# Optimization experiments

Hardware: AMD Instinct MI355X
Metric: run time of the kernel (lower is better)

Reference implementation:

```python
import jax, jax.numpy as jnp
import numpy as np

HID = 64      # HIDDEN_DIM
VOCAB = 64    # VOCAB_SIZE
INNER = 24    # INNER_DIM
SEQ = 32      # SEQ_LEN
CAP = 8       # CAPACITY_LIMIT (deque maxlen)
LR = 0.05     # INFERENCE_LR
B1, B2, EPS = 0.9, 0.999, 1e-8   # torch Adam defaults
LN_EPS = 1e-5                    # torch LayerNorm default
BATCH = 8192


def setup_inputs() -> dict:
    key = jax.random.key(0)
    ks = jax.random.split(key, 8)
    def w(k, shape, s=0.02):
        return jax.random.normal(k, shape, jnp.float32) * s
    return {
        "seqs": jax.random.randint(ks[0], (BATCH, SEQ), 0, VOCAB, dtype=jnp.int32),
        "embed": w(ks[1], (VOCAB, HID), 1.0),
        "ff_w1": w(ks[2], (HID, 2 * HID)), "ff_b1": jnp.zeros((2 * HID,), jnp.float32),
        "ff_w2": w(ks[3], (2 * HID, HID)), "ff_b2": jnp.zeros((HID,), jnp.float32),
        "ln_g": jnp.ones((HID,), jnp.float32), "ln_b": jnp.zeros((HID,), jnp.float32),
        "mlp_w1": w(ks[4], (HID, INNER), 0.1), "mlp_b1": jnp.zeros((INNER,), jnp.float32),
        "mlp_w2": w(ks[5], (INNER, HID), 0.1), "mlp_b2": jnp.zeros((HID,), jnp.float32),
        "out_w": w(ks[6], (HID, VOCAB)), "out_b": jnp.zeros((VOCAB,), jnp.float32),
    }


def _mlp(p, x):
    w1, b1, w2, b2 = p
    return jnp.maximum(x @ w1 + b1, 0.0) @ w2 + b2


def reference(seqs, embed, ff_w1, ff_b1, ff_w2, ff_b2, ln_g, ln_b,
              mlp_w1, mlp_b1, mlp_w2, mlp_b2, out_w, out_b):
    # Encoder over all tokens used (t = 0..SEQ-2), batched: [B, 31, HID]
    h = embed[seqs[:, : SEQ - 1]]
    f = jnp.maximum(h @ ff_w1 + ff_b1, 0.0) @ ff_w2 + ff_b2
    x = h + f
    mu = x.mean(-1, keepdims=True)
    var = ((x - mu) ** 2).mean(-1, keepdims=True)
    enc = ln_g * (x - mu) * jax.lax.rsqrt(var + LN_EPS) + ln_b

    # deque(maxlen=8) over pairs (t even -> key, t odd -> val) keeps last 8 pairs:
    # keys at t = 14,16,...,28 ; vals at t = 15,17,...,29. Entries are detached.
    keys = jax.lax.stop_gradient(enc[:, 14:29:2])  # [B, 8, HID]
    vals = jax.lax.stop_gradient(enc[:, 15:30:2])  # [B, 8, HID]
    q = enc[:, SEQ - 2]                            # [B, HID]

    # load_state_dict copy breaks the graph -> base MLP params are constants here
    p0 = tuple(jax.lax.stop_gradient(p) for p in (mlp_w1, mlp_b1, mlp_w2, mlp_b2))
    steps = jnp.arange(1, CAP + 1, dtype=jnp.float32)

    def per_sample(k_i, v_i, q_i):
        def adam_step(carry, kv):
            p, m, v = carry
            kh, vh, t = kv
            g = jax.grad(lambda pp: jnp.mean((_mlp(pp, kh) - vh) ** 2))(p)
            m = jax.tree_util.tree_map(lambda a, b: B1 * a + (1.0 - B1) * b, m, g)
            v = jax.tree_util.tree_map(lambda a, b: B2 * a + (1.0 - B2) * b * b, v, g)
            bc1 = 1.0 - B1 ** t
            bc2 = 1.0 - B2 ** t
            p = jax.tree_util.tree_map(
                lambda pp, mm, vv: pp - LR * (mm / bc1) / (jnp.sqrt(vv / bc2) + EPS),
                p, m, v)
            return (p, m, v), None
        zeros = jax.tree_util.tree_map(jnp.zeros_like, p0)
        (pT, _, _), _ = jax.lax.scan(adam_step, (p0, zeros, zeros), (k_i, v_i, steps))
        return _mlp(pT, q_i)

    hq = jax.vmap(per_sample)(keys, vals, q)   # [B, HID]
    return hq @ out_w + out_b                  # [B, VOCAB]
```

## Files before the change

### kernel.cpp

```cpp
#include <hip/hip_runtime.h>
#include <hip/hip_bf16.h>
#include <math.h>

#define HID   64
#define VOCABN 64
#define INNER 24
#define SEQN  32
#define CAPN  8
#define NPOS  17
#define BATCHN 8192

typedef float f32x4 __attribute__((ext_vector_type(4)));
typedef float f32x2 __attribute__((ext_vector_type(2)));

static __device__ __forceinline__ f32x2 pk_fma2(f32x2 a, f32x2 b, f32x2 c) {
  f32x2 r; r.x = fmaf(a.x, b.x, c.x); r.y = fmaf(a.y, b.y, c.y); return r;
}
static __device__ __forceinline__ f32x2 pk_max2(f32x2 a, f32x2 b) {
  f32x2 r; r.x = fmaxf(a.x, b.x); r.y = fmaxf(a.y, b.y); return r;
}
static __device__ __forceinline__ f32x2 sp2(float x) { return (f32x2){x, x}; }

static __device__ const float CMSBR[8] = {
  0.01581139f, 0.01176584f, 0.01010053f, 0.00918844f,
  0.00862495f, 0.00825540f, 0.00800653f, 0.00783856f
};

__device__ __forceinline__ float allred32(float x) {
  int y;
  y = __builtin_amdgcn_update_dpp(__float_as_int(x), __float_as_int(x),
                                  0xB1, 0xF, 0xF, false);
  x += __int_as_float(y);
  y = __builtin_amdgcn_update_dpp(__float_as_int(x), __float_as_int(x),
                                  0x4E, 0xF, 0xF, false);
  x += __int_as_float(y);
  x += __int_as_float(__builtin_amdgcn_ds_swizzle(__float_as_int(x), 0x101F));
  x += __int_as_float(__builtin_amdgcn_ds_swizzle(__float_as_int(x), 0x201F));
  x += __int_as_float(__builtin_amdgcn_ds_swizzle(__float_as_int(x), 0x401F));
  return x;
}

__global__ __launch_bounds__(128) void build_table(
    const float* __restrict__ embed,
    const float* __restrict__ ff_w1,
    const float* __restrict__ ff_b1,
    const float* __restrict__ ff_w2,
    const float* __restrict__ ff_b2,
    const float* __restrict__ ln_g,
    const float* __restrict__ ln_b,
    float* __restrict__ etab)
{
  __shared__ float h[64];
  __shared__ float A1[128];
  __shared__ float xs[64];
  const int r = blockIdx.x;
  const int t = threadIdx.x;

  if (t < 64) h[t] = embed[r * 64 + t];
  __syncthreads();

  {
    float acc = ff_b1[t];
    #pragma unroll 8
    for (int k = 0; k < 64; ++k)
      acc = fmaf(h[k], ff_w1[k * 128 + t], acc);
    A1[t] = fmaxf(acc, 0.f);
  }
  __syncthreads();

  if (t < 64) {
    float acc = ff_b2[t];
    #pragma unroll 8
    for (int k = 0; k < 128; ++k)
      acc = fmaf(A1[k], ff_w2[k * 64 + t], acc);
    xs[t] = acc + h[t];
  }
  __syncthreads();

  if (t < 64) {
    float s1 = 0.f;
    if (t < 4)
      for (int j = 0; j < 16; ++j) s1 += xs[t + 4 * j];
    s1 += __shfl_xor(s1, 1);
    s1 += __shfl_xor(s1, 2);
    s1 = __shfl(s1, 0);
    float mu = s1 * 0.015625f;

    float s2 = 0.f;
    if (t < 4)
      for (int j = 0; j < 16; ++j) {
        float d = xs[t + 4 * j] - mu;
        s2 = fmaf(d, d, s2);
      }
    s2 += __shfl_xor(s2, 1);
    s2 += __shfl_xor(s2, 2);
    s2 = __shfl(s2, 0);
    float var = s2 * 0.015625f;
    float rs  = rsqrtf(var + 1e-5f);

    etab[r * 64 + t] = fmaf((xs[t] - mu) * rs, ln_g[t], ln_b[t]);
  }
}

__device__ __forceinline__ void adam_pk(f32x2& p, f32x2& m, f32x2& v,
                                        f32x2 g1, f32x2 g2, float cmsbr) {
  m = pk_fma2(sp2(0.9f),   m, g1);
  v = pk_fma2(sp2(0.999f), v, g2);
  f32x2 vc = pk_max2(v, sp2(1e-30f));
  f32x2 r; r.x = __builtin_amdgcn_rsqf(vc.x); r.y = __builtin_amdgcn_rsqf(vc.y);
  f32x2 t = m * sp2(cmsbr);
  p = pk_fma2(-t, r, p);
}

__global__ __launch_bounds__(256, 2) void adapt_kernel(
    const int* __restrict__ seqs,
    const float* __restrict__ etab,
    const float* __restrict__ mlp_w1,
    const float* __restrict__ mlp_b1,
    const float* __restrict__ mlp_w2,
    const float* __restrict__ mlp_b2,
    const float* __restrict__ out_w,
    const float* __restrict__ out_b,
    float* __restrict__ out)
{
  __shared__ __align__(16) float hqv[4][64];
  const int t    = threadIdx.x;
  const int wv   = t >> 6;
  const int lane = t & 63;
  const int h    = lane >> 5;
  const int u    = lane & 31;
  const int s    = blockIdx.x * 4 + wv;
  const int off  = 12 * h;

  const int* __restrict__ srow = seqs + s * SEQN + 14;

  f32x2 w1[12], m1[12], v1[12], w2[12], m2[12], v2[12];
  #pragma unroll
  for (int m = 0; m < 12; ++m) {
    f32x2 a; a.x = mlp_w1[(2 * u) * INNER + off + m];
             a.y = mlp_w1[(2 * u + 1) * INNER + off + m];
    w1[m] = a;
    w2[m] = *(const f32x2*)&mlp_w2[(off + m) * HID + 2 * u];
    m1[m] = sp2(0.f); v1[m] = sp2(0.f); m2[m] = sp2(0.f); v2[m] = sp2(0.f);
  }
  const bool own1 = (u < 6);
  f32x2 b1v = own1 ? *(const f32x2*)&mlp_b1[off + 2 * u] : sp2(0.f);
  f32x2 mb1 = sp2(0.f), vb1 = sp2(0.f);
  f32x2 b2v = (h == 0) ? *(const f32x2*)&mlp_b2[2 * u] : sp2(0.f);
  f32x2 mb2 = sp2(0.f), vb2 = sp2(0.f);

  const bool ou0 = (u == 0), ou1 = (u == 1), ou2 = (u == 2);
  const bool ou3 = (u == 3), ou4 = (u == 4), ou5 = (u == 5);

  const f32x2* e2 = (const f32x2*)etab;
  f32x2 kp = e2[srow[0] * 32 + u];
  f32x2 vp = e2[srow[1] * 32 + u];

  #pragma unroll 1
  for (int st = 0; st < 8; ++st) {
    const float cmsbr = CMSBR[st];

    f32x2 pz[12];
    #pragma unroll
    for (int m = 0; m < 12; ++m) pz[m] = kp * w1[m];
    pz[0].x  += ou0 ? b1v.x : 0.f;  pz[1].y  += ou0 ? b1v.y : 0.f;
    pz[2].x  += ou1 ? b1v.x : 0.f;  pz[3].y  += ou1 ? b1v.y : 0.f;
    pz[4].x  += ou2 ? b1v.x : 0.f;  pz[5].y  += ou2 ? b1v.y : 0.f;
    pz[6].x  += ou3 ? b1v.x : 0.f;  pz[7].y  += ou3 ? b1v.y : 0.f;
    pz[8].x  += ou4 ? b1v.x : 0.f;  pz[9].y  += ou4 ? b1v.y : 0.f;
    pz[10].x += ou5 ? b1v.x : 0.f;  pz[11].y += ou5 ? b1v.y : 0.f;
    float a_[12];
    #pragma unroll
    for (int m = 0; m < 12; ++m) a_[m] = allred32(pz[m].x + pz[m].y);
    #pragma unroll
    for (int m = 0; m < 12; ++m) a_[m] = fmaxf(a_[m], 0.f);

    f32x2 qA = (h == 0) ? b2v : sp2(0.f);
    #pragma unroll
    for (int m = 0; m < 6; ++m)  qA = pk_fma2(sp2(a_[m]), w2[m], qA);
    f32x2 qB = sp2(0.f);
    #pragma unroll
    for (int m = 6; m < 12; ++m) qB = pk_fma2(sp2(a_[m]), w2[m], qB);
    f32x2 sH = qA + qB;
    f32x2 sO; sO.x = __shfl_xor(sH.x, 32); sO.y = __shfl_xor(sH.y, 32);
    f32x2 ys  = sH + sO;
    f32x2 dyv = (ys - vp) * sp2(0.03125f);

    int pp1 = 2 * st + 2; pp1 = pp1 < 16 ? pp1 : 16;
    int pp2 = 2 * st + 3; pp2 = pp2 < 16 ? pp2 : 16;
    f32x2 kn = e2[srow[pp1] * 32 + u];
    f32x2 vn = e2[srow[pp2] * 32 + u];

    float dz[12];
    #pragma unroll
    for (int m = 0; m < 12; ++m) {
      f32x2 bb = w2[m] * dyv;
      dz[m] = allred32(bb.x + bb.y);
    }
    #pragma unroll
    for (int m = 0; m < 12; ++m) dz[m] = (a_[m] > 0.f) ? dz[m] : 0.f;

    f32x2 k01  = kp * sp2(0.1f);
    f32x2 ksq  = (sp2(0.001f) * kp) * kp;
    f32x2 dy01 = dyv * sp2(0.1f);
    f32x2 dysq = (sp2(0.001f) * dyv) * dyv;
    #pragma unroll
    for (int m = 0; m < 12; ++m) {
      float dzs = dz[m] * dz[m];
      adam_pk(w1[m], m1[m], v1[m], k01 * sp2(dz[m]), ksq * sp2(dzs), cmsbr);
      float as = a_[m] * a_[m];
      adam_pk(w2[m], m2[m], v2[m], dy01 * sp2(a_[m]), dysq * sp2(as), cmsbr);
    }
    float glo = ou0 ? dz[0] : ou1 ? dz[2] : ou2 ? dz[4]
              : ou3 ? dz[6] : ou4 ? dz[8] : dz[10];
    float ghi = ou0 ? dz[1] : ou1 ? dz[3] : ou2 ? dz[5]
              : ou3 ? dz[7] : ou4 ? dz[9] : dz[11];
    f32x2 g1b; g1b.x = 0.1f * glo;           g1b.y = 0.1f * ghi;
    f32x2 g2b; g2b.x = 0.001f * (glo * glo); g2b.y = 0.001f * (ghi * ghi);
    adam_pk(b1v, mb1, vb1, g1b, g2b, cmsbr);
    adam_pk(b2v, mb2, vb2, dy01, dysq, cmsbr);

    kp = kn; vp = vn;
  }

  {
    f32x2 pz[12];
    #pragma unroll
    for (int m = 0; m < 12; ++m) pz[m] = kp * w1[m];
    pz[0].x  += ou0 ? b1v.x : 0.f;  pz[1].y  += ou0 ? b1v.y : 0.f;
    pz[2].x  += ou1 ? b1v.x : 0.f;  pz[3].y  += ou1 ? b1v.y : 0.f;
    pz[4].x  += ou2 ? b1v.x : 0.f;  pz[5].y  += ou2 ? b1v.y : 0.f;
    pz[6].x  += ou3 ? b1v.x : 0.f;  pz[7].y  += ou3 ? b1v.y : 0.f;
    pz[8].x  += ou4 ? b1v.x : 0.f;  pz[9].y  += ou4 ? b1v.y : 0.f;
    pz[10].x += ou5 ? b1v.x : 0.f;  pz[11].y += ou5 ? b1v.y : 0.f;
    float aq[12];
    #pragma unroll
    for (int m = 0; m < 12; ++m) aq[m] = fmaxf(allred32(pz[m].x + pz[m].y), 0.f);
    f32x2 qA = (h == 0) ? b2v : sp2(0.f);
    #pragma unroll
    for (int m = 0; m < 6; ++m)  qA = pk_fma2(sp2(aq[m]), w2[m], qA);
    f32x2 qB = sp2(0.f);
    #pragma unroll
    for (int m = 6; m < 12; ++m) qB = pk_fma2(sp2(aq[m]), w2[m], qB);
    f32x2 sH = qA + qB;
    f32x2 sO; sO.x = __shfl_xor(sH.x, 32); sO.y = __shfl_xor(sH.y, 32);
    f32x2 hq = sH + sO;
    if (h == 0) *(f32x2*)&hqv[wv][2 * u] = hq;
  }
  __syncthreads();

  {
    float acc = out_b[lane];
    const f32x4* hv = (const f32x4*)hqv[wv];
    #pragma unroll
    for (int j4 = 0; j4 < 16; ++j4) {
      f32x4 h4 = hv[j4];
      acc = fmaf(h4.x, out_w[(4 * j4 + 0) * 64 + lane], acc);
      acc = fmaf(h4.y, out_w[(4 * j4 + 1) * 64 + lane], acc);
      acc = fmaf(h4.z, out_w[(4 * j4 + 2) * 64 + lane], acc);
      acc = fmaf(h4.w, out_w[(4 * j4 + 3) * 64 + lane], acc);
    }
    out[(size_t)s * 64 + lane] = acc;
  }
}

extern "C" void kernel_launch(void* const* d_in, const int* in_sizes, int n_in,
                              void* d_out, int out_size, void* d_ws, size_t ws_size,
                              hipStream_t stream) {
  const int*   seqs   = (const int*)d_in[0];
  const float* embed  = (const float*)d_in[1];
  const float* ff_w1  = (const float*)d_in[2];
  const float* ff_b1  = (const float*)d_in[3];
  const float* ff_w2  = (const float*)d_in[4];
  const float* ff_b2  = (const float*)d_in[5];
  const float* ln_g   = (const float*)d_in[6];
  const float* ln_b   = (const float*)d_in[7];
  const float* mlp_w1 = (const float*)d_in[8];
  const float* mlp_b1 = (const float*)d_in[9];
  const float* mlp_w2 = (const float*)d_in[10];
  const float* mlp_b2 = (const float*)d_in[11];
  const float* out_w  = (const float*)d_in[12];
  const float* out_b  = (const float*)d_in[13];

  float* etab = (float*)d_ws;

  build_table<<<64, 128, 0, stream>>>(
      embed, ff_w1, ff_b1, ff_w2, ff_b2, ln_g, ln_b, etab);
  adapt_kernel<<<BATCHN / 4, 256, 0, stream>>>(
      seqs, etab, mlp_w1, mlp_b1, mlp_w2, mlp_b2, out_w, out_b,
      (float*)d_out);
}
```

Baseline: 179.7 us.

## Remap wave work to four 16-lane groups each owning 4 hidden elements

Changes the per-sample wave decomposition from two 32-lane halves (2 hidden elements per lane, 12 inner units each) to four 16-lane groups (4 hidden elements per lane, 6 inner units each). Each cross-lane reduction now spans 16 lanes instead of 32, dropping one swizzle step per reduction and halving the number of reductions per lane. The output recombination needs an extra swizzle plus shuffle across groups, and bias ownership logic becomes more intricate. Per-lane register state for Adam stays about the same.

```diff
diff --git a/kernel.cpp b/kernel.cpp
--- a/kernel.cpp
+++ b/kernel.cpp
@@ -13,20 +13,32 @@
 typedef float f32x4 __attribute__((ext_vector_type(4)));
 typedef float f32x2 __attribute__((ext_vector_type(2)));
 
-static __device__ __forceinline__ f32x2 pk_fma2(f32x2 a, f32x2 b, f32x2 c) {
-  f32x2 r; r.x = fmaf(a.x, b.x, c.x); r.y = fmaf(a.y, b.y, c.y); return r;
-}
-static __device__ __forceinline__ f32x2 pk_max2(f32x2 a, f32x2 b) {
-  f32x2 r; r.x = fmaxf(a.x, b.x); r.y = fmaxf(a.y, b.y); return r;
-}
-static __device__ __forceinline__ f32x2 sp2(float x) { return (f32x2){x, x}; }
+static __device__ __forceinline__ f32x4 sp4(float x) { return (f32x4){x, x, x, x}; }
+static __device__ __forceinline__ f32x4 fma4(f32x4 a, f32x4 b, f32x4 c) {
+  f32x4 r; r.x = fmaf(a.x, b.x, c.x); r.y = fmaf(a.y, b.y, c.y);
+           r.z = fmaf(a.z, b.z, c.z); r.w = fmaf(a.w, b.w, c.w); return r;
+}
+static __device__ __forceinline__ f32x4 max4(f32x4 a, float b) {
+  f32x4 r; r.x = fmaxf(a.x, b); r.y = fmaxf(a.y, b);
+           r.z = fmaxf(a.z, b); r.w = fmaxf(a.w, b); return r;
+}
+static __device__ __forceinline__ f32x4 rsq4(f32x4 a) {
+  f32x4 r; r.x = __builtin_amdgcn_rsqf(a.x); r.y = __builtin_amdgcn_rsqf(a.y);
+           r.z = __builtin_amdgcn_rsqf(a.z); r.w = __builtin_amdgcn_rsqf(a.w); return r;
+}
 
 static __device__ const float CMSBR[8] = {
   0.01581139f, 0.01176584f, 0.01010053f, 0.00918844f,
   0.00862495f, 0.00825540f, 0.00800653f, 0.00783856f
 };
 
-__device__ __forceinline__ float allred32(float x) {
+template <int PAT>
+static __device__ __forceinline__ float swz(float x) {
+  return __int_as_float(__builtin_amdgcn_ds_swizzle(__float_as_int(x), PAT));
+}
+
+__device__ __forceinline__ float allred16q(f32x4 p) {
+  float x = (p.x + p.y) + (p.z + p.w);
   int y;
   y = __builtin_amdgcn_update_dpp(__float_as_int(x), __float_as_int(x),
                                   0xB1, 0xF, 0xF, false);
@@ -34,9 +46,8 @@
   y = __builtin_amdgcn_update_dpp(__float_as_int(x), __float_as_int(x),
                                   0x4E, 0xF, 0xF, false);
   x += __int_as_float(y);
-  x += __int_as_float(__builtin_amdgcn_ds_swizzle(__float_as_int(x), 0x101F));
-  x += __int_as_float(__builtin_amdgcn_ds_swizzle(__float_as_int(x), 0x201F));
-  x += __int_as_float(__builtin_amdgcn_ds_swizzle(__float_as_int(x), 0x401F));
+  x += swz<0x101F>(x);
+  x += swz<0x201F>(x);
   return x;
 }
 
@@ -102,14 +113,13 @@
   }
 }
 
-__device__ __forceinline__ void adam_pk(f32x2& p, f32x2& m, f32x2& v,
-                                        f32x2 g1, f32x2 g2, float cmsbr) {
-  m = pk_fma2(sp2(0.9f),   m, g1);
-  v = pk_fma2(sp2(0.999f), v, g2);
-  f32x2 vc = pk_max2(v, sp2(1e-30f));
-  f32x2 r; r.x = __builtin_amdgcn_rsqf(vc.x); r.y = __builtin_amdgcn_rsqf(vc.y);
-  f32x2 t = m * sp2(cmsbr);
-  p = pk_fma2(-t, r, p);
+__device__ __forceinline__ void adam_q(f32x4& p, f32x4& m, f32x4& v,
+                                       f32x4 g1, f32x4 g2, float cmsbr) {
+  m = fma4(sp4(0.9f),   m, g1);
+  v = fma4(sp4(0.999f), v, g2);
+  f32x4 r = rsq4(max4(v, 1e-30f));
+  f32x4 t = m * sp4(cmsbr);
+  p = fma4(-t, r, p);
 }
 
 __global__ __launch_bounds__(256, 2) void adapt_kernel(
@@ -127,125 +137,142 @@
   const int t    = threadIdx.x;
   const int wv   = t >> 6;
   const int lane = t & 63;
-  const int h    = lane >> 5;
-  const int u    = lane & 31;
+  const int g    = lane >> 4;
+  const int u16  = lane & 15;
   const int s    = blockIdx.x * 4 + wv;
-  const int off  = 12 * h;
+  const int off  = 6 * g;
 
   const int* __restrict__ srow = seqs + s * SEQN + 14;
 
-  f32x2 w1[12], m1[12], v1[12], w2[12], m2[12], v2[12];
+  f32x4 w1q[6], m1q[6], v1q[6], w2q[6], m2q[6], v2q[6];
   #pragma unroll
-  for (int m = 0; m < 12; ++m) {
-    f32x2 a; a.x = mlp_w1[(2 * u) * INNER + off + m];
-             a.y = mlp_w1[(2 * u + 1) * INNER + off + m];
-    w1[m] = a;
-    w2[m] = *(const f32x2*)&mlp_w2[(off + m) * HID + 2 * u];
-    m1[m] = sp2(0.f); v1[m] = sp2(0.f); m2[m] = sp2(0.f); v2[m] = sp2(0.f);
-  }
-  const bool own1 = (u < 6);
-  f32x2 b1v = own1 ? *(const f32x2*)&mlp_b1[off + 2 * u] : sp2(0.f);
-  f32x2 mb1 = sp2(0.f), vb1 = sp2(0.f);
-  f32x2 b2v = (h == 0) ? *(const f32x2*)&mlp_b2[2 * u] : sp2(0.f);
-  f32x2 mb2 = sp2(0.f), vb2 = sp2(0.f);
-
-  const bool ou0 = (u == 0), ou1 = (u == 1), ou2 = (u == 2);
-  const bool ou3 = (u == 3), ou4 = (u == 4), ou5 = (u == 5);
-
-  const f32x2* e2 = (const f32x2*)etab;
-  f32x2 kp = e2[srow[0] * 32 + u];
-  f32x2 vp = e2[srow[1] * 32 + u];
+  for (int m = 0; m < 6; ++m) {
+    f32x4 a;
+    a.x = mlp_w1[(4 * u16 + 0) * INNER + off + m];
+    a.y = mlp_w1[(4 * u16 + 1) * INNER + off + m];
+    a.z = mlp_w1[(4 * u16 + 2) * INNER + off + m];
+    a.w = mlp_w1[(4 * u16 + 3) * INNER + off + m];
+    w1q[m] = a;
+    w2q[m] = *(const f32x4*)&mlp_w2[(off + m) * HID + 4 * u16];
+    m1q[m] = sp4(0.f); v1q[m] = sp4(0.f); m2q[m] = sp4(0.f); v2q[m] = sp4(0.f);
+  }
+  f32x4 b1q = sp4(0.f);
+  if (!(g & 1)) {
+    if (u16 == 0) { b1q.x = mlp_b1[off + 0]; b1q.y = mlp_b1[off + 1];
+                    b1q.z = mlp_b1[off + 2]; b1q.w = mlp_b1[off + 3]; }
+    else if (u16 == 1) { b1q.x = mlp_b1[off + 4]; b1q.y = mlp_b1[off + 5]; }
+  } else {
+    if (u16 == 1) { b1q.z = mlp_b1[off + 0]; b1q.w = mlp_b1[off + 1]; }
+    else if (u16 == 2) { b1q.x = mlp_b1[off + 2]; b1q.y = mlp_b1[off + 3];
+                         b1q.z = mlp_b1[off + 4]; b1q.w = mlp_b1[off + 5]; }
+  }
+  f32x4 mb1 = sp4(0.f), vb1 = sp4(0.f);
+  f32x4 b2q = *(const f32x4*)&mlp_b2[4 * u16];
+  f32x4 mb2 = sp4(0.f), vb2 = sp4(0.f);
+
+  const bool ge0 = !(g & 1) && (u16 == 0);
+  const bool ge1 = !(g & 1) && (u16 == 1);
+  const bool go1 =  (g & 1) && (u16 == 1);
+  const bool go2 =  (g & 1) && (u16 == 2);
+  const bool g0a = (g == 0);
+
+  const f32x4* e4 = (const f32x4*)etab;
+  f32x4 kp = e4[srow[0] * 16 + u16];
+  f32x4 vp = e4[srow[1] * 16 + u16];
 
   #pragma unroll 1
   for (int st = 0; st < 8; ++st) {
     const float cmsbr = CMSBR[st];
 
-    f32x2 pz[12];
-    #pragma unroll
-    for (int m = 0; m < 12; ++m) pz[m] = kp * w1[m];
-    pz[0].x  += ou0 ? b1v.x : 0.f;  pz[1].y  += ou0 ? b1v.y : 0.f;
-    pz[2].x  += ou1 ? b1v.x : 0.f;  pz[3].y  += ou1 ? b1v.y : 0.f;
-    pz[4].x  += ou2 ? b1v.x : 0.f;  pz[5].y  += ou2 ? b1v.y : 0.f;
-    pz[6].x  += ou3 ? b1v.x : 0.f;  pz[7].y  += ou3 ? b1v.y : 0.f;
-    pz[8].x  += ou4 ? b1v.x : 0.f;  pz[9].y  += ou4 ? b1v.y : 0.f;
-    pz[10].x += ou5 ? b1v.x : 0.f;  pz[11].y += ou5 ? b1v.y : 0.f;
-    float a_[12];
-    #pragma unroll
-    for (int m = 0; m < 12; ++m) a_[m] = allred32(pz[m].x + pz[m].y);
-    #pragma unroll
-    for (int m = 0; m < 12; ++m) a_[m] = fmaxf(a_[m], 0.f);
-
-    f32x2 qA = (h == 0) ? b2v : sp2(0.f);
-    #pragma unroll
-    for (int m = 0; m < 6; ++m)  qA = pk_fma2(sp2(a_[m]), w2[m], qA);
-    f32x2 qB = sp2(0.f);
-    #pragma unroll
-    for (int m = 6; m < 12; ++m) qB = pk_fma2(sp2(a_[m]), w2[m], qB);
-    f32x2 sH = qA + qB;
-    f32x2 sO; sO.x = __shfl_xor(sH.x, 32); sO.y = __shfl_xor(sH.y, 32);
-    f32x2 ys  = sH + sO;
-    f32x2 dyv = (ys - vp) * sp2(0.03125f);
+    f32x4 pz[6];
+    #pragma unroll
+    for (int m = 0; m < 6; ++m) pz[m] = kp * w1q[m];
+    pz[0].x += ge0 ? b1q.x : 0.f;  pz[0].z += go1 ? b1q.z : 0.f;
+    pz[1].y += ge0 ? b1q.y : 0.f;  pz[1].w += go1 ? b1q.w : 0.f;
+    pz[2].z += ge0 ? b1q.z : 0.f;  pz[2].x += go2 ? b1q.x : 0.f;
+    pz[3].w += ge0 ? b1q.w : 0.f;  pz[3].y += go2 ? b1q.y : 0.f;
+    pz[4].x += ge1 ? b1q.x : 0.f;  pz[4].z += go2 ? b1q.z : 0.f;
+    pz[5].y += ge1 ? b1q.y : 0.f;  pz[5].w += go2 ? b1q.w : 0.f;
+    float a_[6];
+    #pragma unroll
+    for (int m = 0; m < 6; ++m) a_[m] = allred16q(pz[m]);
+    #pragma unroll
+    for (int m = 0; m < 6; ++m) a_[m] = fmaxf(a_[m], 0.f);
+
+    f32x4 yq;
+    yq.x = g0a ? b2q.x : 0.f; yq.y = g0a ? b2q.y : 0.f;
+    yq.z = g0a ? b2q.z : 0.f; yq.w = g0a ? b2q.w : 0.f;
+    #pragma unroll
+    for (int m = 0; m < 6; ++m) yq = fma4(sp4(a_[m]), w2q[m], yq);
+    { f32x4 e; e.x = swz<0x401F>(yq.x); e.y = swz<0x401F>(yq.y);
+               e.z = swz<0x401F>(yq.z); e.w = swz<0x401F>(yq.w);
+      yq = yq + e; }
+    { f32x4 e; e.x = __shfl_xor(yq.x, 32); e.y = __shfl_xor(yq.y, 32);
+               e.z = __shfl_xor(yq.z, 32); e.w = __shfl_xor(yq.w, 32);
+      yq = yq + e; }
+    f32x4 dyq = (yq - vp) * sp4(0.03125f);
 
     int pp1 = 2 * st + 2; pp1 = pp1 < 16 ? pp1 : 16;
     int pp2 = 2 * st + 3; pp2 = pp2 < 16 ? pp2 : 16;
-    f32x2 kn = e2[srow[pp1] * 32 + u];
-    f32x2 vn = e2[srow[pp2] * 32 + u];
-
-    float dz[12];
-    #pragma unroll
-    for (int m = 0; m < 12; ++m) {
-      f32x2 bb = w2[m] * dyv;
-      dz[m] = allred32(bb.x + bb.y);
+    f32x4 kn = e4[srow[pp1] * 16 + u16];
+    f32x4 vn = e4[srow[pp2] * 16 + u16];
+
+    float dz[6];
+    #pragma unroll
+    for (int m = 0; m < 6; ++m) dz[m] = allred16q(w2q[m] * dyq);
+    #pragma unroll
+    for (int m = 0; m < 6; ++m) dz[m] = (a_[m] > 0.f) ? dz[m] : 0.f;
+
+    f32x4 k01  = kp * sp4(0.1f);
+    f32x4 ksq  = (sp4(0.001f) * kp) * kp;
+    f32x4 dy01 = dyq * sp4(0.1f);
+    f32x4 dysq = (sp4(0.001f) * dyq) * dyq;
+    #pragma unroll
+    for (int m = 0; m < 6; ++m) {
+      float dzs = dz[m] * dz[m];
+      adam_q(w1q[m], m1q[m], v1q[m], k01 * sp4(dz[m]), ksq * sp4(dzs), cmsbr);
+      float as = a_[m] * a_[m];
+      adam_q(w2q[m], m2q[m], v2q[m], dy01 * sp4(a_[m]), dysq * sp4(as), cmsbr);
     }
-    #pragma unroll
-    for (int m = 0; m < 12; ++m) dz[m] = (a_[m] > 0.f) ? dz[m] : 0.f;
-
-    f32x2 k01  = kp * sp2(0.1f);
-    f32x2 ksq  = (sp2(0.001f) * kp) * kp;
-    f32x2 dy01 = dyv * sp2(0.1f);
-    f32x2 dysq = (sp2(0.001f) * dyv) * dyv;
-    #pragma unroll
-    for (int m = 0; m < 12; ++m) {
-      float dzs = dz[m] * dz[m];
-      adam_pk(w1[m], m1[m], v1[m], k01 * sp2(dz[m]), ksq * sp2(dzs), cmsbr);
-      float as = a_[m] * a_[m];
-      adam_pk(w2[m], m2[m], v2[m], dy01 * sp2(a_[m]), dysq * sp2(as), cmsbr);
-    }
-    float glo = ou0 ? dz[0] : ou1 ? dz[2] : ou2 ? dz[4]
-              : ou3 ? dz[6] : ou4 ? dz[8] : dz[10];
-    float ghi = ou0 ? dz[1] : ou1 ? dz[3] : ou2 ? dz[5]
-              : ou3 ? dz[7] : ou4 ? dz[9] : dz[11];
-    f32x2 g1b; g1b.x = 0.1f * glo;           g1b.y = 0.1f * ghi;
-    f32x2 g2b; g2b.x = 0.001f * (glo * glo); g2b.y = 0.001f * (ghi * ghi);
-    adam_pk(b1v, mb1, vb1, g1b, g2b, cmsbr);
-    adam_pk(b2v, mb2, vb2, dy01, dysq, cmsbr);
+    float gg0 = ge0 ? dz[0] : ge1 ? dz[4] : dz[2];
+    float gg1 = ge0 ? dz[1] : ge1 ? dz[5] : dz[3];
+    float gg2 = go1 ? dz[0] : ge0 ? dz[2] : dz[4];
+    float gg3 = go1 ? dz[1] : ge0 ? dz[3] : dz[5];
+    f32x4 g1b; g1b.x = 0.1f * gg0; g1b.y = 0.1f * gg1;
+               g1b.z = 0.1f * gg2; g1b.w = 0.1f * gg3;
+    f32x4 g2b; g2b.x = 0.001f * (gg0 * gg0); g2b.y = 0.001f * (gg1 * gg1);
+               g2b.z = 0.001f * (gg2 * gg2); g2b.w = 0.001f * (gg3 * gg3);
+    adam_q(b1q, mb1, vb1, g1b, g2b, cmsbr);
+    adam_q(b2q, mb2, vb2, dy01, dysq, cmsbr);
 
     kp = kn; vp = vn;
   }
 
   {
-    f32x2 pz[12];
-    #pragma unroll
-    for (int m = 0; m < 12; ++m) pz[m] = kp * w1[m];
-    pz[0].x  += ou0 ? b1v.x : 0.f;  pz[1].y  += ou0 ? b1v.y : 0.f;
-    pz[2].x  += ou1 ? b1v.x : 0.f;  pz[3].y  += ou1 ? b1v.y : 0.f;
-    pz[4].x  += ou2 ? b1v.x : 0.f;  pz[5].y  += ou2 ? b1v.y : 0.f;
-    pz[6].x  += ou3 ? b1v.x : 0.f;  pz[7].y  += ou3 ? b1v.y : 0.f;
-    pz[8].x  += ou4 ? b1v.x : 0.f;  pz[9].y  += ou4 ? b1v.y : 0.f;
-    pz[10].x += ou5 ? b1v.x : 0.f;  pz[11].y += ou5 ? b1v.y : 0.f;
-    float aq[12];
-    #pragma unroll
-    for (int m = 0; m < 12; ++m) aq[m] = fmaxf(allred32(pz[m].x + pz[m].y), 0.f);
-    f32x2 qA = (h == 0) ? b2v : sp2(0.f);
-    #pragma unroll
-    for (int m = 0; m < 6; ++m)  qA = pk_fma2(sp2(aq[m]), w2[m], qA);
-    f32x2 qB = sp2(0.f);
-    #pragma unroll
-    for (int m = 6; m < 12; ++m) qB = pk_fma2(sp2(aq[m]), w2[m], qB);
-    f32x2 sH = qA + qB;
-    f32x2 sO; sO.x = __shfl_xor(sH.x, 32); sO.y = __shfl_xor(sH.y, 32);
-    f32x2 hq = sH + sO;
-    if (h == 0) *(f32x2*)&hqv[wv][2 * u] = hq;
+    f32x4 pz[6];
+    #pragma unroll
+    for (int m = 0; m < 6; ++m) pz[m] = kp * w1q[m];
+    pz[0].x += ge0 ? b1q.x : 0.f;  pz[0].z += go1 ? b1q.z : 0.f;
+    pz[1].y += ge0 ? b1q.y : 0.f;  pz[1].w += go1 ? b1q.w : 0.f;
+    pz[2].z += ge0 ? b1q.z : 0.f;  pz[2].x += go2 ? b1q.x : 0.f;
+    pz[3].w += ge0 ? b1q.w : 0.f;  pz[3].y += go2 ? b1q.y : 0.f;
+    pz[4].x += ge1 ? b1q.x : 0.f;  pz[4].z += go2 ? b1q.z : 0.f;
+    pz[5].y += ge1 ? b1q.y : 0.f;  pz[5].w += go2 ? b1q.w : 0.f;
+    float aq[6];
+    #pragma unroll
+    for (int m = 0; m < 6; ++m) aq[m] = fmaxf(allred16q(pz[m]), 0.f);
+    f32x4 hq;
+    hq.x = g0a ? b2q.x : 0.f; hq.y = g0a ? b2q.y : 0.f;
+    hq.z = g0a ? b2q.z : 0.f; hq.w = g0a ? b2q.w : 0.f;
+    #pragma unroll
+    for (int m = 0; m < 6; ++m) hq = fma4(sp4(aq[m]), w2q[m], hq);
+    { f32x4 e; e.x = swz<0x401F>(hq.x); e.y = swz<0x401F>(hq.y);
+               e.z = swz<0x401F>(hq.z); e.w = swz<0x401F>(hq.w);
+      hq = hq + e; }
+    { f32x4 e; e.x = __shfl_xor(hq.x, 32); e.y = __shfl_xor(hq.y, 32);
+               e.z = __shfl_xor(hq.z, 32); e.w = __shfl_xor(hq.w, 32);
+      hq = hq + e; }
+    if (g0a) ((f32x4*)hqv[wv])[u16] = hq;
   }
   __syncthreads();
 
```

New measurement: 170.8 us. 1.05x faster.
